# Kernel tuning notes

Hardware: AMD Instinct MI355X
Metric: run time of the kernel (lower is better)

The kernel has to match this reference:

```python
import jax, jax.numpy as jnp
import numpy as np

B, CIN, CP, H, W = 64, 256, 128, 32, 32
EPS = 1e-5


def conv1x1(x, w, b):
    # x: [B,C,H,W], w: [O,C], b: [O]
    return jnp.einsum('bchw,oc->bohw', x, w) + b[None, :, None, None]


def batchnorm(x, g, beta):
    # training-mode BatchNorm2d (batch stats over B,H,W; biased variance)
    m = x.mean(axis=(0, 2, 3), keepdims=True)
    v = x.var(axis=(0, 2, 3), keepdims=True)
    return (x - m) * jax.lax.rsqrt(v + EPS) * g[None, :, None, None] + beta[None, :, None, None]


def setup_inputs() -> dict:
    key = jax.random.key(0)
    ks = jax.random.split(key, 5)
    s = 0.05  # keep pre-softmax logits in a sane range
    d = {
        'x': jax.random.normal(ks[0], (B, CIN, H, W), jnp.float32),
        'theta_w': jax.random.normal(ks[1], (CP, CIN), jnp.float32) * s,
        'theta_b': jnp.zeros((CP,), jnp.float32),
        'theta_g': jnp.ones((CP,), jnp.float32),
        'theta_beta': jnp.zeros((CP,), jnp.float32),
        'phi_w': jax.random.normal(ks[2], (CP, CIN), jnp.float32) * s,
        'phi_b': jnp.zeros((CP,), jnp.float32),
        'phi_g': jnp.ones((CP,), jnp.float32),
        'phi_beta': jnp.zeros((CP,), jnp.float32),
        'gamma_w': jax.random.normal(ks[3], (CP, CIN), jnp.float32) * s,
        'gamma_b': jnp.zeros((CP,), jnp.float32),
        'gamma_g': jnp.ones((CP,), jnp.float32),
        'gamma_beta': jnp.zeros((CP,), jnp.float32),
        'omega_w': jax.random.normal(ks[4], (CIN, CP), jnp.float32) * s,
        'omega_b': jnp.zeros((CIN,), jnp.float32),
        'omega_g': jnp.ones((CIN,), jnp.float32),
        'omega_beta': jnp.zeros((CIN,), jnp.float32),
    }
    return d


def reference(x, theta_w, theta_b, theta_g, theta_beta,
              phi_w, phi_b, phi_g, phi_beta,
              gamma_w, gamma_b, gamma_g, gamma_beta,
              omega_w, omega_b, omega_g, omega_beta):
    b, c, h, w = x.shape
    n = h * w
    t = batchnorm(conv1x1(x, theta_w, theta_b), theta_g, theta_beta).reshape(b, -1, n)  # [B,CP,N]
    p = batchnorm(conv1x1(x, phi_w, phi_b), phi_g, phi_beta).reshape(b, -1, n)          # [B,CP,N]
    g = batchnorm(conv1x1(x, gamma_w, gamma_b), gamma_g, gamma_beta).reshape(b, -1, n)  # [B,CP,N]
    # attention = t^T @ p : [B,N,N]
    attn = jnp.einsum('bcn,bcm->bnm', t, p)
    # whole-matrix softmax (normalize over all N*N entries per batch element)
    attn = jax.nn.softmax(attn.reshape(b, -1), axis=1).reshape(b, n, n)
    # sat = attn @ g^T, kept channels-first: [B,CP,N]
    sat = jnp.einsum('bnm,bcm->bcn', attn, g).reshape(b, -1, h, w)
    sat = batchnorm(conv1x1(sat, omega_w, omega_b), omega_g, omega_beta)
    return x + sat
```

## Files before the change

### kernel.cpp

```cpp
#include <hip/hip_runtime.h>
#include <cstdio>


typedef __attribute__((ext_vector_type(4))) float f32x4;
typedef __attribute__((ext_vector_type(8))) short short8;
typedef __attribute__((ext_vector_type(4))) unsigned short u16x4;
typedef __attribute__((ext_vector_type(8))) unsigned short u16x8;
typedef __attribute__((ext_vector_type(4))) int i32x4;

static constexpr float CEXP = 40.0f;
static constexpr float LOG2E = 1.4426950408889634f;

static constexpr long OFF_WST  = 0;
static constexpr long OFF_VEC  = 147456;
static constexpr long OFF_R1   = 148608;
static constexpr long OFF_R2   = 149376;
static constexpr long OFF_ZS   = 149888;
static constexpr long OFF_SC1  = 149952;
static constexpr long OFF_SH1  = 150336;
static constexpr long OFF_SC2  = 150720;
static constexpr long OFF_SH2  = 150976;
static constexpr long OFF_INVZ = 151232;
static constexpr long OFF_OM   = 151296;
static constexpr long OFF_X    = 262144;
static constexpr long OFF_Y    = OFF_X + 16777216;
static constexpr long OFF_C    = OFF_Y + 25165824;
static constexpr long OFF_D    = OFF_C + 4194304;
static constexpr long WS_FLOATS = OFF_D + 4194304;

__device__ __forceinline__ unsigned short f2bf(float f) {
    union { float f; unsigned u; } x; x.f = f;
    unsigned r = x.u + 0x7FFF + ((x.u >> 16) & 1);
    return (unsigned short)(r >> 16);
}
__device__ __forceinline__ float bf2f(unsigned short h) {
    union { unsigned u; float f; } x; x.u = ((unsigned)h) << 16; return x.f;
}
__device__ __forceinline__ void glds16(const void* g, void* l) {
    __builtin_amdgcn_global_load_lds(
        (const __attribute__((address_space(1))) unsigned int*)g,
        (__attribute__((address_space(3))) unsigned int*)l, 16, 0, 0);
}

__global__ void zero_n(float* p, int n) {
    int i = blockIdx.x * 256 + threadIdx.x;
    if (i < n) p[i] = 0.f;
}

__global__ void invz_kernel(const float* zs, float* invz) {
    int i = threadIdx.x;
    if (i < 64) invz[i] = 1.0f / zs[i];
}

__global__ void stack_params(const float* tw, const float* tb, const float* tg, const float* tbe,
                             const float* pw, const float* pb, const float* pg, const float* pbe,
                             const float* gw, const float* gb, const float* gg, const float* gbe,
                             const float* ow,
                             unsigned short* Wsp, float* vecs, unsigned short* omB) {
    int i = blockIdx.x * 256 + threadIdx.x;
    if (i < 98304) {
        int o = i >> 8, c = i & 255;
        float v = (o < 128) ? tw[o * 256 + c] : (o < 256) ? pw[(o - 128) * 256 + c]
                                                          : gw[(o - 256) * 256 + c];
        unsigned short hi = f2bf(v);
        unsigned short lo = f2bf(v - bf2f(hi));
        Wsp[(long)o * 768 + c] = hi;
        Wsp[(long)o * 768 + 256 + c] = lo;
        Wsp[(long)o * 768 + 512 + c] = hi;
    }
    if (i < 32768) omB[i] = f2bf(ow[i]);
    if (i < 384) {
        float b  = (i < 128) ? tb[i]  : (i < 256) ? pb[i - 128]  : gb[i - 256];
        float g  = (i < 128) ? tg[i]  : (i < 256) ? pg[i - 128]  : gg[i - 256];
        float be = (i < 128) ? tbe[i] : (i < 256) ? pbe[i - 128] : gbe[i - 256];
        vecs[i] = b; vecs[384 + i] = g; vecs[768 + i] = be;
    }
}

__global__ __launch_bounds__(256) void transpose_x(const float* __restrict__ x,
                                                   unsigned short* __restrict__ xs) {
    __shared__ float t[64][68];
    const int b = blockIdx.z, c0 = blockIdx.y * 64, n0 = blockIdx.x * 64;
    const int tid = threadIdx.x;
#pragma unroll
    for (int p = 0; p < 4; ++p) {
        int i = tid + p * 256;
        int c = i >> 4, n4 = (i & 15) << 2;
        f32x4 v = *(const f32x4*)&x[((long)b * 256 + c0 + c) * 1024 + n0 + n4];
        *(f32x4*)&t[c][n4] = v;
    }
    __syncthreads();
#pragma unroll
    for (int p = 0; p < 4; ++p) {
        int i = tid + p * 256;
        int n = i >> 4, c4 = (i & 15) << 2;
        u16x4 h, l;
#pragma unroll
        for (int j = 0; j < 4; ++j) {
            float v = t[c4 + j][n];
            unsigned short hh = f2bf(v);
            h[j] = hh;
            l[j] = f2bf(v - bf2f(hh));
        }
        long o = ((long)b * 1024 + n0 + n) * 512 + c0 + c4;
        *(u16x4*)&xs[o] = h;
        *(u16x4*)&xs[o + 256] = l;
    }
}

template <int NT, bool OUT_BF16, bool HAS_CBIAS, bool CSTAT, bool EXPZ>
__global__ __launch_bounds__(512) void mgemm8(
    int gx, int gy,
    const unsigned short* __restrict__ A, long aBatch, long aOff, int lda,
    int athr, int adlo, int adhi,
    const unsigned short* __restrict__ B, long bBatch, long bOff, int ldb,
    int bthr, int bdlo, int bdhi,
    void* __restrict__ Cq, long cBatch, int ldc,
    const float* __restrict__ bias, float* __restrict__ stats, int statStride,
    float* __restrict__ zsum) {
    constexpr int AU = 256 * 64;
    constexpr int BU = 128 * 64;
    constexpr int BUFU = AU + BU;
    __shared__ unsigned short lds[3 * BUFU];

    const int nwg = gridDim.x, bid = blockIdx.x;
    const int wk = ((bid & 7) * (nwg >> 3)) + (bid >> 3);
    const int bx = wk % gx;
    const int byz = wk / gx;
    const int by = byz % gy;
    const int z = byz / gy;

    const int tid = threadIdx.x;
    const int wave = tid >> 6, lane = tid & 63;
    const int wm = wave >> 1, wn = wave & 1;
    const int lr = lane & 15, lg = lane >> 4;
    const int m0 = by * 256, n0 = bx * 128;
    const long aB = aOff + (long)z * aBatch;
    const long bB = bOff + (long)z * bBatch;
    const int grow = lane >> 3, gq = lane & 7;

    f32x4 acc[4][4];
#pragma unroll
    for (int i = 0; i < 4; ++i)
#pragma unroll
        for (int j = 0; j < 4; ++j) acc[i][j] = (f32x4){0.f, 0.f, 0.f, 0.f};

    auto stageA = [&](int buf, int kt, int t) {
        const int ka = (kt < athr ? kt + adlo : kt + adhi);
        int seg = wave + t * 8;
        int row = seg * 8 + grow;
        glds16(A + aB + (long)(m0 + row) * lda + ka + ((gq ^ (row & 7)) << 3),
               &lds[buf + seg * 512]);
    };
    auto stageB = [&](int buf, int kt, int t) {
        const int kb = (kt < bthr ? kt + bdlo : kt + bdhi);
        int seg = wave + t * 8;
        int row = seg * 8 + grow;
        glds16(B + bB + (long)(n0 + row) * ldb + kb + ((gq ^ (row & 7)) << 3),
               &lds[buf + AU + seg * 512]);
    };
    auto stage_all = [&](int buf, int kt) {
#pragma unroll
        for (int t = 0; t < 4; ++t) stageA(buf, kt, t);
#pragma unroll
        for (int t = 0; t < 2; ++t) stageB(buf, kt, t);
    };

    stage_all(0, 0);
    if (NT > 1) stage_all(BUFU, 64);

#pragma unroll
    for (int t = 0; t < NT; ++t) {
        const unsigned bb = (unsigned)(((t % 3) * BUFU) * 2);
        if (t + 1 < NT) asm volatile("s_waitcnt vmcnt(6)" ::: "memory");
        else            asm volatile("s_waitcnt vmcnt(0)" ::: "memory");
        asm volatile("s_barrier" ::: "memory");
        const int sbuf = ((t + 2) % 3) * BUFU;
        const int skt = (t + 2) * 64;
#pragma unroll
        for (int p = 0; p < 2; ++p) {
            i32x4 a4[4], b4[4];
#pragma unroll
            for (int mi = 0; mi < 4; ++mi) {
                unsigned r = (unsigned)(wm * 64 + mi * 16 + lr);
                unsigned ad = bb + r * 128 + ((unsigned)(((p << 2) | lg) ^ (r & 7)) << 4);
                asm volatile("ds_read_b128 %0, %1" : "=v"(a4[mi]) : "v"(ad));
            }
#pragma unroll
            for (int ni = 0; ni < 4; ++ni) {
                unsigned r = (unsigned)(wn * 64 + ni * 16 + lr);
                unsigned ad = bb + (unsigned)(AU * 2) + r * 128 +
                              ((unsigned)(((p << 2) | lg) ^ (r & 7)) << 4);
                asm volatile("ds_read_b128 %0, %1" : "=v"(b4[ni]) : "v"(ad));
            }
            if (t + 2 < NT) {
                if (p == 0) { stageA(sbuf, skt, 0); stageA(sbuf, skt, 1); stageA(sbuf, skt, 2); }
                else        { stageA(sbuf, skt, 3); stageB(sbuf, skt, 0); stageB(sbuf, skt, 1); }
            }
            asm volatile("s_waitcnt lgkmcnt(0)" ::: "memory");
            __builtin_amdgcn_sched_barrier(0);
            __builtin_amdgcn_s_setprio(1);
#pragma unroll
            for (int ni = 0; ni < 4; ++ni) {
                short8 bh = __builtin_bit_cast(short8, b4[ni]);
#pragma unroll
                for (int mi = 0; mi < 4; ++mi)
                    acc[mi][ni] = __builtin_amdgcn_mfma_f32_16x16x32_bf16(
                        __builtin_bit_cast(short8, a4[mi]), bh, acc[mi][ni], 0, 0, 0);
            }
            __builtin_amdgcn_s_setprio(0);
            if (p == 0) asm volatile("s_barrier" ::: "memory");
        }
    }

    float cb[4];
#pragma unroll
    for (int ni = 0; ni < 4; ++ni)
        cb[ni] = HAS_CBIAS ? bias[n0 + wn * 64 + ni * 16 + lr] : 0.0f;

    if constexpr (OUT_BF16) {
        __syncthreads();
        unsigned short* tileH = lds;
        float zacc = 0.f;
#pragma unroll
        for (int mi = 0; mi < 4; ++mi) {
            const int lrow = wm * 64 + mi * 16 + lg * 4;
#pragma unroll
            for (int ni = 0; ni < 4; ++ni) {
                const int cl = wn * 64 + ni * 16 + lr;
                f32x4 v = acc[mi][ni] + (f32x4){cb[ni], cb[ni], cb[ni], cb[ni]};
#pragma unroll
                for (int j = 0; j < 4; ++j) {
                    unsigned short o;
                    if constexpr (EXPZ) {
                        float e = exp2f((v[j] - CEXP) * LOG2E);
                        o = f2bf(e);
                        zacc += bf2f(o);
                    } else {
                        o = f2bf(v[j]);
                    }
                    tileH[(lrow + j) * 128 + cl] = o;
                }
            }
        }
        __syncthreads();
#pragma unroll
        for (int i = tid; i < 256 * 128 / 8; i += 512) {
            int row = i >> 4, c8 = (i & 15) << 3;
            u16x8 vv = *(const u16x8*)&tileH[row * 128 + c8];
            *(u16x8*)&((unsigned short*)Cq)[(long)z * cBatch + (long)(m0 + row) * ldc + n0 + c8] = vv;
        }
        if constexpr (EXPZ) {
            __syncthreads();
            float* red = (float*)lds;
            red[tid] = zacc;
            __syncthreads();
            for (int o = 256; o > 0; o >>= 1) {
                if (tid < o) red[tid] += red[tid + o];
                __syncthreads();
            }
            if (tid == 0) atomicAdd(&zsum[z], red[0]);
        }
    } else {
        float* tileF = (float*)lds;
        float scol[4] = {0.f, 0.f, 0.f, 0.f}, s2col[4] = {0.f, 0.f, 0.f, 0.f};
#pragma unroll
        for (int pass = 0; pass < 2; ++pass) {
            __syncthreads();
            if ((wm >> 1) == pass) {
#pragma unroll
                for (int mi = 0; mi < 4; ++mi) {
                    const int lrow = (wm & 1) * 64 + mi * 16 + lg * 4;
#pragma unroll
                    for (int ni = 0; ni < 4; ++ni) {
                        const int cl = wn * 64 + ni * 16 + lr;
                        f32x4 v = acc[mi][ni] + (f32x4){cb[ni], cb[ni], cb[ni], cb[ni]};
                        if constexpr (CSTAT) {
                            scol[ni] += v[0] + v[1] + v[2] + v[3];
                            s2col[ni] += v[0] * v[0] + v[1] * v[1] + v[2] * v[2] + v[3] * v[3];
                        }
#pragma unroll
                        for (int j = 0; j < 4; ++j) tileF[(lrow + j) * 128 + cl] = v[j];
                    }
                }
            }
            __syncthreads();
#pragma unroll
            for (int i = tid; i < 128 * 128 / 4; i += 512) {
                int row = i >> 5, c4 = (i & 31) << 2;
                f32x4 vv = *(const f32x4*)&tileF[row * 128 + c4];
                *(f32x4*)&((float*)Cq)[(long)z * cBatch +
                                       (long)(m0 + pass * 128 + row) * ldc + n0 + c4] = vv;
            }
        }
        if constexpr (CSTAT) {
#pragma unroll
            for (int ni = 0; ni < 4; ++ni) {
                float a = scol[ni], b2 = s2col[ni];
                a += __shfl_xor(a, 16); a += __shfl_xor(a, 32);
                b2 += __shfl_xor(b2, 16); b2 += __shfl_xor(b2, 32);
                if (lg == 0) {
                    const int col = n0 + wn * 64 + ni * 16 + lr;
                    atomicAdd(&stats[col], a);
                    atomicAdd(&stats[statStride + col], b2);
                }
            }
        }
    }
}

template <int NF, int KTOT, bool OUT_BF16, bool HAS_BIAS, bool HAS_CBIAS, bool HAS_SCALE,
          bool RSTAT, bool CSTAT, bool EXPZ>
__global__ __launch_bounds__(256) void mgemm(
    int gx, int gy,
    const unsigned short* __restrict__ A, long aBatch, long aOff, int lda,
    int athr, int adlo, int adhi,
    const unsigned short* __restrict__ B, long bBatch, long bOff, int ldb,
    int bthr, int bdlo, int bdhi,
    void* __restrict__ Cq, long cBatch, int ldc,
    const float* __restrict__ bias, const float* __restrict__ bscale,
    float* __restrict__ stats, int statStride, float* __restrict__ zsum) {
    constexpr int AU = 128 * 32;
    constexpr int BU = NF * 32 * 32;
    constexpr int BUFU = AU + BU;
    constexpr int S = KTOT / 32;
    constexpr int LPS = 2 + NF / 2;
    constexpr int COLS = NF * 32;
    __shared__ unsigned short lds[4 * BUFU];

    const int nwg = gridDim.x;
    const int bid = blockIdx.x;
    const int wk = ((bid & 7) * (nwg >> 3)) + (bid >> 3);
    const int bx = wk % gx;
    const int byz = wk / gx;
    const int by = byz % gy;
    const int z = byz / gy;

    const int tid = threadIdx.x;
    const int wave = tid >> 6, lane = tid & 63;
    const int wm = wave >> 1, wn = wave & 1;
    const int lr = lane & 15, lg = lane >> 4;
    const int m0 = by * 128, n0 = bx * COLS;
    const long aB = aOff + (long)z * aBatch;
    const long bB = bOff + (long)z * bBatch;
    const int srow = lane >> 2;
    const int sq   = lane & 3;

    f32x4 acc[4][NF];
#pragma unroll
    for (int i = 0; i < 4; ++i)
#pragma unroll
        for (int j = 0; j < NF; ++j) acc[i][j] = (f32x4){0.f, 0.f, 0.f, 0.f};

    auto stage = [&](int bufu, int kt) {
        const int ka = (kt < athr ? kt + adlo : kt + adhi);
        const int kb = (kt < bthr ? kt + bdlo : kt + bdhi);
#pragma unroll
        for (int t = 0; t < 2; ++t) {
            int seg = wave + t * 4;
            int row = seg * 16 + srow;
            int gq = sq ^ ((row >> 1) & 3);
            glds16(A + aB + (long)(m0 + row) * lda + ka + gq * 8, &lds[bufu + seg * 512]);
        }
#pragma unroll
        for (int t = 0; t < NF / 2; ++t) {
            int seg = wave + t * 4;
            int row = seg * 16 + srow;
            int gq = sq ^ ((row >> 1) & 3);
            glds16(B + bB + (long)(n0 + row) * ldb + kb + gq * 8, &lds[bufu + AU + seg * 512]);
        }
    };

    stage(0, 0);
    stage(BUFU, 32);
    stage(2 * BUFU, 64);

#pragma unroll
    for (int s = 0; s < S; ++s) {
        const int bufu = (s & 3) * BUFU;
        const unsigned bb = (unsigned)(bufu * 2);
        const int rem = (S - 1 - s) < 2 ? (S - 1 - s) : 2;
        if (rem == 2)      asm volatile("s_waitcnt vmcnt(%0)" ::"i"(2 * LPS) : "memory");
        else if (rem == 1) asm volatile("s_waitcnt vmcnt(%0)" ::"i"(LPS) : "memory");
        else               asm volatile("s_waitcnt vmcnt(0)" ::: "memory");
        asm volatile("s_barrier" ::: "memory");
        i32x4 a4[4], b4[NF];
#pragma unroll
        for (int mi = 0; mi < 4; ++mi) {
            unsigned r = (unsigned)(wm * 64 + mi * 16 + lr);
            unsigned ad = bb + r * 64 + ((unsigned)(lg ^ ((r >> 1) & 3)) * 16);
            asm volatile("ds_read_b128 %0, %1" : "=v"(a4[mi]) : "v"(ad));
        }
#pragma unroll
        for (int ni = 0; ni < NF; ++ni) {
            unsigned r = (unsigned)(wn * NF * 16 + ni * 16 + lr);
            unsigned ad = bb + (unsigned)(AU * 2) + r * 64 + ((unsigned)(lg ^ ((r >> 1) & 3)) * 16);
            asm volatile("ds_read_b128 %0, %1" : "=v"(b4[ni]) : "v"(ad));
        }
        if (s + 3 < S) stage(((s + 3) & 3) * BUFU, (s + 3) * 32);
        asm volatile("s_waitcnt lgkmcnt(0)" ::: "memory");
        __builtin_amdgcn_sched_barrier(0);
        __builtin_amdgcn_s_setprio(1);
#pragma unroll
        for (int ni = 0; ni < NF; ++ni) {
            short8 bh = __builtin_bit_cast(short8, b4[ni]);
#pragma unroll
            for (int mi = 0; mi < 4; ++mi)
                acc[mi][ni] = __builtin_amdgcn_mfma_f32_16x16x32_bf16(
                    __builtin_bit_cast(short8, a4[mi]), bh, acc[mi][ni], 0, 0, 0);
        }
        __builtin_amdgcn_s_setprio(0);
    }

    __syncthreads();
    const float sc = HAS_SCALE ? bscale[z] : 1.0f;
    float zacc = 0.f;
    float scol[NF], s2col[NF];
    if constexpr (CSTAT) {
#pragma unroll
        for (int ni = 0; ni < NF; ++ni) { scol[ni] = 0.f; s2col[ni] = 0.f; }
    }
    unsigned short* tileH = lds;
    float* tileF = (float*)lds;
#pragma unroll
    for (int mi = 0; mi < 4; ++mi) {
        const int mrow = m0 + wm * 64 + mi * 16 + lg * 4;
        const int lrow = wm * 64 + mi * 16 + lg * 4;
        f32x4 bi = (f32x4){0.f, 0.f, 0.f, 0.f};
        if constexpr (HAS_BIAS) bi = *(const f32x4*)&bias[mrow];
        f32x4 s = (f32x4){0.f, 0.f, 0.f, 0.f}, s2 = s;
#pragma unroll
        for (int ni = 0; ni < NF; ++ni) {
            const int cl = wn * NF * 16 + ni * 16 + lr;
            f32x4 v = acc[mi][ni] * sc + bi;
            if constexpr (HAS_CBIAS) {
                float bc = bias[n0 + cl];
                v += (f32x4){bc, bc, bc, bc};
            }
            if constexpr (RSTAT) { s += v; s2 += v * v; }
            if constexpr (CSTAT) {
                scol[ni] += v[0] + v[1] + v[2] + v[3];
                s2col[ni] += v[0] * v[0] + v[1] * v[1] + v[2] * v[2] + v[3] * v[3];
            }
            if constexpr (OUT_BF16) {
#pragma unroll
                for (int j = 0; j < 4; ++j) {
                    unsigned short o;
                    if constexpr (EXPZ) {
                        float e = exp2f((v[j] - CEXP) * LOG2E);
                        o = f2bf(e);
                        zacc += bf2f(o);
                    } else {
                        o = f2bf(v[j]);
                    }
                    tileH[(lrow + j) * COLS + cl] = o;
                }
            } else {
#pragma unroll
                for (int j = 0; j < 4; ++j) tileF[(lrow + j) * COLS + cl] = v[j];
            }
        }
        if constexpr (RSTAT) {
#pragma unroll
            for (int m = 1; m < 16; m <<= 1) {
#pragma unroll
                for (int r = 0; r < 4; ++r) {
                    s[r] += __shfl_xor(s[r], m);
                    s2[r] += __shfl_xor(s2[r], m);
                }
            }
            if (lr == 0) {
#pragma unroll
                for (int r = 0; r < 4; ++r) {
                    atomicAdd(&stats[mrow + r], s[r]);
                    atomicAdd(&stats[statStride + mrow + r], s2[r]);
                }
            }
        }
    }
    if constexpr (CSTAT) {
#pragma unroll
        for (int ni = 0; ni < NF; ++ni) {
            float a = scol[ni], b2 = s2col[ni];
            a += __shfl_xor(a, 16); a += __shfl_xor(a, 32);
            b2 += __shfl_xor(b2, 16); b2 += __shfl_xor(b2, 32);
            if (lg == 0) {
                const int col = n0 + wn * NF * 16 + ni * 16 + lr;
                atomicAdd(&stats[col], a);
                atomicAdd(&stats[statStride + col], b2);
            }
        }
    }
    __syncthreads();
    if constexpr (OUT_BF16) {
#pragma unroll
        for (int i = tid; i < 128 * COLS / 8; i += 256) {
            int row = i / (COLS / 8), c8 = (i % (COLS / 8)) * 8;
            u16x8 vv = *(const u16x8*)&tileH[row * COLS + c8];
            *(u16x8*)&((unsigned short*)Cq)[(long)z * cBatch + (long)(m0 + row) * ldc + n0 + c8] = vv;
        }
    } else {
#pragma unroll
        for (int i = tid; i < 128 * COLS / 4; i += 256) {
            int row = i / (COLS / 4), c4 = (i % (COLS / 4)) * 4;
            f32x4 vv = *(const f32x4*)&tileF[row * COLS + c4];
            *(f32x4*)&((float*)Cq)[(long)z * cBatch + (long)(m0 + row) * ldc + n0 + c4] = vv;
        }
    }
    if constexpr (EXPZ) {
        __syncthreads();
        float* red = (float*)lds;
        red[tid] = zacc;
        __syncthreads();
        for (int o = 128; o > 0; o >>= 1) {
            if (tid < o) red[tid] += red[tid + o];
            __syncthreads();
        }
        if (tid == 0) atomicAdd(&zsum[z], red[0]);
    }
}

__global__ void finalize_stats(const float* __restrict__ raw, int n, int stride,
                               const float* __restrict__ g, const float* __restrict__ beta,
                               float* __restrict__ osc, float* __restrict__ osh) {
    int ch = blockIdx.x * 256 + threadIdx.x;
    if (ch < n) {
        double mean = (double)raw[ch] / 65536.0;
        double var = (double)raw[stride + ch] / 65536.0 - mean * mean;
        double s = (double)g[ch] / sqrt(var + 1e-5);
        osc[ch] = (float)s;
        osh[ch] = (float)((double)beta[ch] - mean * s);
    }
}

__global__ __launch_bounds__(256) void norm_tp(const float* __restrict__ YT,
                                               const float* __restrict__ sc,
                                               const float* __restrict__ sh,
                                               unsigned short* __restrict__ tps) {
    const long total = 64L * 1024 * 64;
    for (long idx = (long)blockIdx.x * 256 + threadIdx.x; idx < total;
         idx += (long)gridDim.x * 256) {
        long row = idx >> 6;
        int cg = (int)(idx & 63) << 2;
        f32x4 v = *(const f32x4*)&YT[row * 384 + cg];
        f32x4 scv = *(const f32x4*)&sc[cg];
        f32x4 shv = *(const f32x4*)&sh[cg];
        v = v * scv + shv;
        u16x4 h, l;
#pragma unroll
        for (int j = 0; j < 4; ++j) {
            unsigned short hh = f2bf(v[j]);
            h[j] = hh;
            l[j] = f2bf(v[j] - bf2f(hh));
        }
        long rb = row * 512;
        if (cg < 128) {
            *(u16x4*)&tps[rb + cg] = h;
            *(u16x4*)&tps[rb + 128 + cg] = l;
        } else {
            *(u16x4*)&tps[rb + 128 + cg] = h;
            *(u16x4*)&tps[rb + 256 + cg] = l;
        }
    }
}

__global__ __launch_bounds__(256) void norm_g(const float* __restrict__ YT,
                                              const float* __restrict__ sc,
                                              const float* __restrict__ sh,
                                              unsigned short* __restrict__ g) {
    __shared__ float t[64][68];
    const int b = blockIdx.z, c0 = blockIdx.y * 64, n0 = blockIdx.x * 64;
    const int tid = threadIdx.x;
#pragma unroll
    for (int p = 0; p < 4; ++p) {
        int i = tid + p * 256;
        int n = i >> 4, c4 = (i & 15) << 2;
        f32x4 v = *(const f32x4*)&YT[((long)b * 1024 + n0 + n) * 384 + 256 + c0 + c4];
        f32x4 scv = *(const f32x4*)&sc[256 + c0 + c4];
        f32x4 shv = *(const f32x4*)&sh[256 + c0 + c4];
        v = v * scv + shv;
        *(f32x4*)&t[n][c4] = v;
    }
    __syncthreads();
#pragma unroll
    for (int p = 0; p < 4; ++p) {
        int i = tid + p * 256;
        int c = i >> 4, n4 = (i & 15) << 2;
        u16x4 o;
#pragma unroll
        for (int j = 0; j < 4; ++j) o[j] = f2bf(t[n4 + j][c]);
        *(u16x4*)&g[((long)b * 128 + c0 + c) * 1024 + n0 + n4] = o;
    }
}

__global__ __launch_bounds__(256) void final_kernel(const float* __restrict__ x,
                                                    const float* __restrict__ out0T,
                                                    const float* __restrict__ sc,
                                                    const float* __restrict__ sh,
                                                    float* __restrict__ out) {
    __shared__ float t[64][68];
    const int b = blockIdx.z, oc0 = blockIdx.y * 64, n0 = blockIdx.x * 64;
    const int tid = threadIdx.x;
#pragma unroll
    for (int p = 0; p < 4; ++p) {
        int i = tid + p * 256;
        int n = i >> 4, c4 = (i & 15) << 2;
        f32x4 v = *(const f32x4*)&out0T[((long)b * 1024 + n0 + n) * 256 + oc0 + c4];
        *(f32x4*)&t[n][c4] = v;
    }
    __syncthreads();
#pragma unroll
    for (int p = 0; p < 4; ++p) {
        int i = tid + p * 256;
        int oc = i >> 4, n4 = (i & 15) << 2;
        const float scv = sc[oc0 + oc], shv = sh[oc0 + oc];
        long o = ((long)b * 256 + oc0 + oc) * 1024 + n0 + n4;
        f32x4 xv = *(const f32x4*)&x[o];
        f32x4 v;
#pragma unroll
        for (int j = 0; j < 4; ++j) v[j] = xv[j] + t[n4 + j][oc] * scv + shv;
        *(f32x4*)&out[o] = v;
    }
}

extern "C" void kernel_launch(void* const* d_in, const int* in_sizes, int n_in,
                              void* d_out, int out_size, void* d_ws, size_t ws_size,
                              hipStream_t stream) {
    const float* x        = (const float*)d_in[0];
    const float* theta_w  = (const float*)d_in[1];
    const float* theta_b  = (const float*)d_in[2];
    const float* theta_g  = (const float*)d_in[3];
    const float* theta_be = (const float*)d_in[4];
    const float* phi_w    = (const float*)d_in[5];
    const float* phi_b    = (const float*)d_in[6];
    const float* phi_g    = (const float*)d_in[7];
    const float* phi_be   = (const float*)d_in[8];
    const float* gamma_w  = (const float*)d_in[9];
    const float* gamma_b  = (const float*)d_in[10];
    const float* gamma_g  = (const float*)d_in[11];
    const float* gamma_be = (const float*)d_in[12];
    const float* omega_w  = (const float*)d_in[13];
    const float* omega_b  = (const float*)d_in[14];
    const float* omega_g  = (const float*)d_in[15];
    const float* omega_be = (const float*)d_in[16];
    float* out = (float*)d_out;

    const size_t need = (size_t)WS_FLOATS * 4;
    if (ws_size < need) {
        fprintf(stderr, "kernel_launch: ws_size %zu < needed %zu\n", ws_size, need);
        return;
    }
    float* ws = (float*)d_ws;
    unsigned short* Wsp = (unsigned short*)(ws + OFF_WST);
    float* vecs = ws + OFF_VEC;
    float* r1   = ws + OFF_R1;
    float* r2   = ws + OFF_R2;
    float* zs   = ws + OFF_ZS;
    float* sc1  = ws + OFF_SC1;
    float* sh1  = ws + OFF_SH1;
    float* sc2  = ws + OFF_SC2;
    float* sh2  = ws + OFF_SH2;
    float* invz = ws + OFF_INVZ;
    unsigned short* omB = (unsigned short*)(ws + OFF_OM);
    unsigned short* xs  = (unsigned short*)(ws + OFF_X);
    unsigned short* tps = (unsigned short*)(ws + OFF_X);
    float* out0T        = ws + OFF_X;
    float* YT           = ws + OFF_Y;
    unsigned short* P   = (unsigned short*)(ws + OFF_Y);
    unsigned short* g   = (unsigned short*)(ws + OFF_C);
    unsigned short* satT= (unsigned short*)(ws + OFF_D);

    const int NOMAP = 1 << 30;

    zero_n<<<6, 256, 0, stream>>>(r1, 1344);
    stack_params<<<384, 256, 0, stream>>>(theta_w, theta_b, theta_g, theta_be,
                                          phi_w, phi_b, phi_g, phi_be,
                                          gamma_w, gamma_b, gamma_g, gamma_be,
                                          omega_w, Wsp, vecs, omB);
    transpose_x<<<dim3(16, 4, 64), 256, 0, stream>>>(x, xs);

    mgemm8<12, false, true, true, false><<<768, 512, 0, stream>>>(
        3, 256,
        xs, 0, 0, 512, 256, 0, -256,
        Wsp, 0, 0, 768, NOMAP, 0, 0,
        YT, 0, 384, vecs, r1, 384, nullptr);
    finalize_stats<<<2, 256, 0, stream>>>(r1, 384, 384, vecs + 384, vecs + 768, sc1, sh1);

    norm_tp<<<4096, 256, 0, stream>>>(YT, sc1, sh1, tps);
    norm_g<<<dim3(16, 2, 64), 256, 0, stream>>>(YT, sc1, sh1, g);

    for (int c = 0; c < 2; ++c) {
        const long b0 = (long)c * 32;
        mgemm8<6, true, false, false, true><<<1024, 512, 0, stream>>>(
            8, 4,
            tps, 524288, b0 * 524288, 512, 128, 0, -128,
            tps, 524288, b0 * 524288, 512, 256, 256, 0,
            P, 1048576, 1024, nullptr, nullptr, 0, zs + b0);

        mgemm<2, 1024, true, false, false, false, false, false, false><<<512, 256, 0, stream>>>(
            2, 8,
            P, 1048576, 0, 1024, NOMAP, 0, 0,
            g, 131072, b0 * 131072, 1024, NOMAP, 0, 0,
            satT + b0 * 131072, 131072, 128, nullptr, nullptr, nullptr, 0, nullptr);
    }
    invz_kernel<<<1, 64, 0, stream>>>(zs, invz);

    mgemm<4, 128, false, false, true, true, false, true, false><<<1024, 256, 0, stream>>>(
        2, 8,
        satT, 131072, 0, 128, NOMAP, 0, 0,
        omB, 0, 0, 128, NOMAP, 0, 0,
        out0T, 262144, 256, omega_b, invz, r2, 256, nullptr);
    finalize_stats<<<1, 256, 0, stream>>>(r2, 256, 256, omega_g, omega_be, sc2, sh2);

    final_kernel<<<dim3(16, 4, 64), 256, 0, stream>>>(x, out0T, sc2, sh2, out);
}
```

Measured before the change: 344.8 us.

## Unify GEMMs on 256x128 mgemm8, drop batch chunking, transpose omega output layout

Removes the older 128-row mgemm kernel and routes the attention-times-g and omega GEMMs through the larger-tile mgemm8, which gains row-bias, scale and row-statistics epilogue options. The two half-batch passes become one launch, so the full P matrix is written to a larger workspace. The omega projection now writes channel-major output, which lets the final residual kernel become a plain elementwise grid-stride loop with no LDS transpose. The aim is fewer launches, better tile reuse and cheaper final fusion, at the cost of more workspace memory and a larger P intermediate living in memory at once.

```diff
diff --git a/kernel.cpp b/kernel.cpp
--- a/kernel.cpp
+++ b/kernel.cpp
@@ -24,7 +24,7 @@
 static constexpr long OFF_OM   = 151296;
 static constexpr long OFF_X    = 262144;
 static constexpr long OFF_Y    = OFF_X + 16777216;
-static constexpr long OFF_C    = OFF_Y + 25165824;
+static constexpr long OFF_C    = OFF_Y + 33554432;
 static constexpr long OFF_D    = OFF_C + 4194304;
 static constexpr long WS_FLOATS = OFF_D + 4194304;
 
@@ -108,7 +108,8 @@
     }
 }
 
-template <int NT, bool OUT_BF16, bool HAS_CBIAS, bool CSTAT, bool EXPZ>
+template <int NT, bool OUT_BF16, bool HAS_RBIAS, bool HAS_CBIAS, bool HAS_SCALE,
+          bool RSTAT, bool CSTAT, bool EXPZ>
 __global__ __launch_bounds__(512) void mgemm8(
     int gx, int gy,
     const unsigned short* __restrict__ A, long aBatch, long aOff, int lda,
@@ -116,8 +117,8 @@
     const unsigned short* __restrict__ B, long bBatch, long bOff, int ldb,
     int bthr, int bdlo, int bdhi,
     void* __restrict__ Cq, long cBatch, int ldc,
-    const float* __restrict__ bias, float* __restrict__ stats, int statStride,
-    float* __restrict__ zsum) {
+    const float* __restrict__ bias, const float* __restrict__ bscale,
+    float* __restrict__ stats, int statStride, float* __restrict__ zsum) {
     constexpr int AU = 256 * 64;
     constexpr int BU = 128 * 64;
     constexpr int BUFU = AU + BU;
@@ -213,10 +214,61 @@
         }
     }
 
-    float cb[4];
-#pragma unroll
-    for (int ni = 0; ni < 4; ++ni)
-        cb[ni] = HAS_CBIAS ? bias[n0 + wn * 64 + ni * 16 + lr] : 0.0f;
+    const float sc = HAS_SCALE ? bscale[z] : 1.0f;
+#pragma unroll
+    for (int mi = 0; mi < 4; ++mi) {
+        const int mrow = m0 + wm * 64 + mi * 16 + lg * 4;
+        f32x4 rb = (f32x4){0.f, 0.f, 0.f, 0.f};
+        if constexpr (HAS_RBIAS) rb = *(const f32x4*)&bias[mrow];
+#pragma unroll
+        for (int ni = 0; ni < 4; ++ni) {
+            float cbv = HAS_CBIAS ? bias[n0 + wn * 64 + ni * 16 + lr] : 0.0f;
+            acc[mi][ni] = acc[mi][ni] * sc + rb + (f32x4){cbv, cbv, cbv, cbv};
+        }
+    }
+    if constexpr (RSTAT) {
+#pragma unroll
+        for (int mi = 0; mi < 4; ++mi) {
+            const int mrow = m0 + wm * 64 + mi * 16 + lg * 4;
+            f32x4 s = (f32x4){0.f, 0.f, 0.f, 0.f}, s2 = s;
+#pragma unroll
+            for (int ni = 0; ni < 4; ++ni) { s += acc[mi][ni]; s2 += acc[mi][ni] * acc[mi][ni]; }
+#pragma unroll
+            for (int m = 1; m < 16; m <<= 1) {
+#pragma unroll
+                for (int r = 0; r < 4; ++r) {
+                    s[r] += __shfl_xor(s[r], m);
+                    s2[r] += __shfl_xor(s2[r], m);
+                }
+            }
+            if (lr == 0) {
+#pragma unroll
+                for (int r = 0; r < 4; ++r) {
+                    atomicAdd(&stats[mrow + r], s[r]);
+                    atomicAdd(&stats[statStride + mrow + r], s2[r]);
+                }
+            }
+        }
+    }
+    if constexpr (CSTAT) {
+#pragma unroll
+        for (int ni = 0; ni < 4; ++ni) {
+            float a = 0.f, b2 = 0.f;
+#pragma unroll
+            for (int mi = 0; mi < 4; ++mi) {
+                f32x4 v = acc[mi][ni];
+                a += v[0] + v[1] + v[2] + v[3];
+                b2 += v[0] * v[0] + v[1] * v[1] + v[2] * v[2] + v[3] * v[3];
+            }
+            a += __shfl_xor(a, 16); a += __shfl_xor(a, 32);
+            b2 += __shfl_xor(b2, 16); b2 += __shfl_xor(b2, 32);
+            if (lg == 0) {
+                const int col = n0 + wn * 64 + ni * 16 + lr;
+                atomicAdd(&stats[col], a);
+                atomicAdd(&stats[statStride + col], b2);
+            }
+        }
+    }
 
     if constexpr (OUT_BF16) {
         __syncthreads();
@@ -228,7 +280,7 @@
 #pragma unroll
             for (int ni = 0; ni < 4; ++ni) {
                 const int cl = wn * 64 + ni * 16 + lr;
-                f32x4 v = acc[mi][ni] + (f32x4){cb[ni], cb[ni], cb[ni], cb[ni]};
+                f32x4 v = acc[mi][ni];
 #pragma unroll
                 for (int j = 0; j < 4; ++j) {
                     unsigned short o;
@@ -263,7 +315,6 @@
         }
     } else {
         float* tileF = (float*)lds;
-        float scol[4] = {0.f, 0.f, 0.f, 0.f}, s2col[4] = {0.f, 0.f, 0.f, 0.f};
 #pragma unroll
         for (int pass = 0; pass < 2; ++pass) {
             __syncthreads();
@@ -274,13 +325,8 @@
 #pragma unroll
                     for (int ni = 0; ni < 4; ++ni) {
                         const int cl = wn * 64 + ni * 16 + lr;
-                        f32x4 v = acc[mi][ni] + (f32x4){cb[ni], cb[ni], cb[ni], cb[ni]};
-                        if constexpr (CSTAT) {
-                            scol[ni] += v[0] + v[1] + v[2] + v[3];
-                            s2col[ni] += v[0] * v[0] + v[1] * v[1] + v[2] * v[2] + v[3] * v[3];
-                        }
-#pragma unroll
-                        for (int j = 0; j < 4; ++j) tileF[(lrow + j) * 128 + cl] = v[j];
+#pragma unroll
+                        for (int j = 0; j < 4; ++j) tileF[(lrow + j) * 128 + cl] = acc[mi][ni][j];
                     }
                 }
             }
@@ -293,230 +339,6 @@
                                        (long)(m0 + pass * 128 + row) * ldc + n0 + c4] = vv;
             }
         }
-        if constexpr (CSTAT) {
-#pragma unroll
-            for (int ni = 0; ni < 4; ++ni) {
-                float a = scol[ni], b2 = s2col[ni];
-                a += __shfl_xor(a, 16); a += __shfl_xor(a, 32);
-                b2 += __shfl_xor(b2, 16); b2 += __shfl_xor(b2, 32);
-                if (lg == 0) {
-                    const int col = n0 + wn * 64 + ni * 16 + lr;
-                    atomicAdd(&stats[col], a);
-                    atomicAdd(&stats[statStride + col], b2);
-                }
-            }
-        }
-    }
-}
-
-template <int NF, int KTOT, bool OUT_BF16, bool HAS_BIAS, bool HAS_CBIAS, bool HAS_SCALE,
-          bool RSTAT, bool CSTAT, bool EXPZ>
-__global__ __launch_bounds__(256) void mgemm(
-    int gx, int gy,
-    const unsigned short* __restrict__ A, long aBatch, long aOff, int lda,
-    int athr, int adlo, int adhi,
-    const unsigned short* __restrict__ B, long bBatch, long bOff, int ldb,
-    int bthr, int bdlo, int bdhi,
-    void* __restrict__ Cq, long cBatch, int ldc,
-    const float* __restrict__ bias, const float* __restrict__ bscale,
-    float* __restrict__ stats, int statStride, float* __restrict__ zsum) {
-    constexpr int AU = 128 * 32;
-    constexpr int BU = NF * 32 * 32;
-    constexpr int BUFU = AU + BU;
-    constexpr int S = KTOT / 32;
-    constexpr int LPS = 2 + NF / 2;
-    constexpr int COLS = NF * 32;
-    __shared__ unsigned short lds[4 * BUFU];
-
-    const int nwg = gridDim.x;
-    const int bid = blockIdx.x;
-    const int wk = ((bid & 7) * (nwg >> 3)) + (bid >> 3);
-    const int bx = wk % gx;
-    const int byz = wk / gx;
-    const int by = byz % gy;
-    const int z = byz / gy;
-
-    const int tid = threadIdx.x;
-    const int wave = tid >> 6, lane = tid & 63;
-    const int wm = wave >> 1, wn = wave & 1;
-    const int lr = lane & 15, lg = lane >> 4;
-    const int m0 = by * 128, n0 = bx * COLS;
-    const long aB = aOff + (long)z * aBatch;
-    const long bB = bOff + (long)z * bBatch;
-    const int srow = lane >> 2;
-    const int sq   = lane & 3;
-
-    f32x4 acc[4][NF];
-#pragma unroll
-    for (int i = 0; i < 4; ++i)
-#pragma unroll
-        for (int j = 0; j < NF; ++j) acc[i][j] = (f32x4){0.f, 0.f, 0.f, 0.f};
-
-    auto stage = [&](int bufu, int kt) {
-        const int ka = (kt < athr ? kt + adlo : kt + adhi);
-        const int kb = (kt < bthr ? kt + bdlo : kt + bdhi);
-#pragma unroll
-        for (int t = 0; t < 2; ++t) {
-            int seg = wave + t * 4;
-            int row = seg * 16 + srow;
-            int gq = sq ^ ((row >> 1) & 3);
-            glds16(A + aB + (long)(m0 + row) * lda + ka + gq * 8, &lds[bufu + seg * 512]);
-        }
-#pragma unroll
-        for (int t = 0; t < NF / 2; ++t) {
-            int seg = wave + t * 4;
-            int row = seg * 16 + srow;
-            int gq = sq ^ ((row >> 1) & 3);
-            glds16(B + bB + (long)(n0 + row) * ldb + kb + gq * 8, &lds[bufu + AU + seg * 512]);
-        }
-    };
-
-    stage(0, 0);
-    stage(BUFU, 32);
-    stage(2 * BUFU, 64);
-
-#pragma unroll
-    for (int s = 0; s < S; ++s) {
-        const int bufu = (s & 3) * BUFU;
-        const unsigned bb = (unsigned)(bufu * 2);
-        const int rem = (S - 1 - s) < 2 ? (S - 1 - s) : 2;
-        if (rem == 2)      asm volatile("s_waitcnt vmcnt(%0)" ::"i"(2 * LPS) : "memory");
-        else if (rem == 1) asm volatile("s_waitcnt vmcnt(%0)" ::"i"(LPS) : "memory");
-        else               asm volatile("s_waitcnt vmcnt(0)" ::: "memory");
-        asm volatile("s_barrier" ::: "memory");
-        i32x4 a4[4], b4[NF];
-#pragma unroll
-        for (int mi = 0; mi < 4; ++mi) {
-            unsigned r = (unsigned)(wm * 64 + mi * 16 + lr);
-            unsigned ad = bb + r * 64 + ((unsigned)(lg ^ ((r >> 1) & 3)) * 16);
-            asm volatile("ds_read_b128 %0, %1" : "=v"(a4[mi]) : "v"(ad));
-        }
-#pragma unroll
-        for (int ni = 0; ni < NF; ++ni) {
-            unsigned r = (unsigned)(wn * NF * 16 + ni * 16 + lr);
-            unsigned ad = bb + (unsigned)(AU * 2) + r * 64 + ((unsigned)(lg ^ ((r >> 1) & 3)) * 16);
-            asm volatile("ds_read_b128 %0, %1" : "=v"(b4[ni]) : "v"(ad));
-        }
-        if (s + 3 < S) stage(((s + 3) & 3) * BUFU, (s + 3) * 32);
-        asm volatile("s_waitcnt lgkmcnt(0)" ::: "memory");
-        __builtin_amdgcn_sched_barrier(0);
-        __builtin_amdgcn_s_setprio(1);
-#pragma unroll
-        for (int ni = 0; ni < NF; ++ni) {
-            short8 bh = __builtin_bit_cast(short8, b4[ni]);
-#pragma unroll
-            for (int mi = 0; mi < 4; ++mi)
-                acc[mi][ni] = __builtin_amdgcn_mfma_f32_16x16x32_bf16(
-                    __builtin_bit_cast(short8, a4[mi]), bh, acc[mi][ni], 0, 0, 0);
-        }
-        __builtin_amdgcn_s_setprio(0);
-    }
-
-    __syncthreads();
-    const float sc = HAS_SCALE ? bscale[z] : 1.0f;
-    float zacc = 0.f;
-    float scol[NF], s2col[NF];
-    if constexpr (CSTAT) {
-#pragma unroll
-        for (int ni = 0; ni < NF; ++ni) { scol[ni] = 0.f; s2col[ni] = 0.f; }
-    }
-    unsigned short* tileH = lds;
-    float* tileF = (float*)lds;
-#pragma unroll
-    for (int mi = 0; mi < 4; ++mi) {
-        const int mrow = m0 + wm * 64 + mi * 16 + lg * 4;
-        const int lrow = wm * 64 + mi * 16 + lg * 4;
-        f32x4 bi = (f32x4){0.f, 0.f, 0.f, 0.f};
-        if constexpr (HAS_BIAS) bi = *(const f32x4*)&bias[mrow];
-        f32x4 s = (f32x4){0.f, 0.f, 0.f, 0.f}, s2 = s;
-#pragma unroll
-        for (int ni = 0; ni < NF; ++ni) {
-            const int cl = wn * NF * 16 + ni * 16 + lr;
-            f32x4 v = acc[mi][ni] * sc + bi;
-            if constexpr (HAS_CBIAS) {
-                float bc = bias[n0 + cl];
-                v += (f32x4){bc, bc, bc, bc};
-            }
-            if constexpr (RSTAT) { s += v; s2 += v * v; }
-            if constexpr (CSTAT) {
-                scol[ni] += v[0] + v[1] + v[2] + v[3];
-                s2col[ni] += v[0] * v[0] + v[1] * v[1] + v[2] * v[2] + v[3] * v[3];
-            }
-            if constexpr (OUT_BF16) {
-#pragma unroll
-                for (int j = 0; j < 4; ++j) {
-                    unsigned short o;
-                    if constexpr (EXPZ) {
-                        float e = exp2f((v[j] - CEXP) * LOG2E);
-                        o = f2bf(e);
-                        zacc += bf2f(o);
-                    } else {
-                        o = f2bf(v[j]);
-                    }
-                    tileH[(lrow + j) * COLS + cl] = o;
-                }
-            } else {
-#pragma unroll
-                for (int j = 0; j < 4; ++j) tileF[(lrow + j) * COLS + cl] = v[j];
-            }
-        }
-        if constexpr (RSTAT) {
-#pragma unroll
-            for (int m = 1; m < 16; m <<= 1) {
-#pragma unroll
-                for (int r = 0; r < 4; ++r) {
-                    s[r] += __shfl_xor(s[r], m);
-                    s2[r] += __shfl_xor(s2[r], m);
-                }
-            }
-            if (lr == 0) {
-#pragma unroll
-                for (int r = 0; r < 4; ++r) {
-                    atomicAdd(&stats[mrow + r], s[r]);
-                    atomicAdd(&stats[statStride + mrow + r], s2[r]);
-                }
-            }
-        }
-    }
-    if constexpr (CSTAT) {
-#pragma unroll
-        for (int ni = 0; ni < NF; ++ni) {
-            float a = scol[ni], b2 = s2col[ni];
-            a += __shfl_xor(a, 16); a += __shfl_xor(a, 32);
-            b2 += __shfl_xor(b2, 16); b2 += __shfl_xor(b2, 32);
-            if (lg == 0) {
-                const int col = n0 + wn * NF * 16 + ni * 16 + lr;
-                atomicAdd(&stats[col], a);
-                atomicAdd(&stats[statStride + col], b2);
-            }
-        }
-    }
-    __syncthreads();
-    if constexpr (OUT_BF16) {
-#pragma unroll
-        for (int i = tid; i < 128 * COLS / 8; i += 256) {
-            int row = i / (COLS / 8), c8 = (i % (COLS / 8)) * 8;
-            u16x8 vv = *(const u16x8*)&tileH[row * COLS + c8];
-            *(u16x8*)&((unsigned short*)Cq)[(long)z * cBatch + (long)(m0 + row) * ldc + n0 + c8] = vv;
-        }
-    } else {
-#pragma unroll
-        for (int i = tid; i < 128 * COLS / 4; i += 256) {
-            int row = i / (COLS / 4), c4 = (i % (COLS / 4)) * 4;
-            f32x4 vv = *(const f32x4*)&tileF[row * COLS + c4];
-            *(f32x4*)&((float*)Cq)[(long)z * cBatch + (long)(m0 + row) * ldc + n0 + c4] = vv;
-        }
-    }
-    if constexpr (EXPZ) {
-        __syncthreads();
-        float* red = (float*)lds;
-        red[tid] = zacc;
-        __syncthreads();
-        for (int o = 128; o > 0; o >>= 1) {
-            if (tid < o) red[tid] += red[tid + o];
-            __syncthreads();
-        }
-        if (tid == 0) atomicAdd(&zsum[z], red[0]);
     }
 }
 
@@ -594,32 +416,25 @@
 }
 
 __global__ __launch_bounds__(256) void final_kernel(const float* __restrict__ x,
-                                                    const float* __restrict__ out0T,
+                                                    const float* __restrict__ out0,
                                                     const float* __restrict__ sc,
                                                     const float* __restrict__ sh,
                                                     float* __restrict__ out) {
-    __shared__ float t[64][68];
-    const int b = blockIdx.z, oc0 = blockIdx.y * 64, n0 = blockIdx.x * 64;
-    const int tid = threadIdx.x;
-#pragma unroll
-    for (int p = 0; p < 4; ++p) {
-        int i = tid + p * 256;
-        int n = i >> 4, c4 = (i & 15) << 2;
-        f32x4 v = *(const f32x4*)&out0T[((long)b * 1024 + n0 + n) * 256 + oc0 + c4];
-        *(f32x4*)&t[n][c4] = v;
-    }
-    __syncthreads();
-#pragma unroll
-    for (int p = 0; p < 4; ++p) {
-        int i = tid + p * 256;
-        int oc = i >> 4, n4 = (i & 15) << 2;
-        const float scv = sc[oc0 + oc], shv = sh[oc0 + oc];
-        long o = ((long)b * 256 + oc0 + oc) * 1024 + n0 + n4;
-        f32x4 xv = *(const f32x4*)&x[o];
+    const long total4 = 64L * 256 * 256;
+    for (long idx = (long)blockIdx.x * 256 + threadIdx.x; idx < total4;
+         idx += (long)gridDim.x * 256) {
+        long e = idx << 2;
+        int n = (int)(e & 1023);
+        long t = e >> 10;
+        int oc = (int)(t & 255);
+        long b = t >> 8;
+        f32x4 xv = *(const f32x4*)&x[e];
+        f32x4 ov = *(const f32x4*)&out0[(long)oc * 65536 + b * 1024 + n];
+        const float scv = sc[oc], shv = sh[oc];
         f32x4 v;
 #pragma unroll
-        for (int j = 0; j < 4; ++j) v[j] = xv[j] + t[n4 + j][oc] * scv + shv;
-        *(f32x4*)&out[o] = v;
+        for (int j = 0; j < 4; ++j) v[j] = xv[j] + ov[j] * scv + shv;
+        *(f32x4*)&out[e] = v;
     }
 }
 
@@ -664,9 +479,9 @@
     unsigned short* omB = (unsigned short*)(ws + OFF_OM);
     unsigned short* xs  = (unsigned short*)(ws + OFF_X);
     unsigned short* tps = (unsigned short*)(ws + OFF_X);
-    float* out0T        = ws + OFF_X;
     float* YT           = ws + OFF_Y;
     unsigned short* P   = (unsigned short*)(ws + OFF_Y);
+    float* out0         = ws + OFF_Y;
     unsigned short* g   = (unsigned short*)(ws + OFF_C);
     unsigned short* satT= (unsigned short*)(ws + OFF_D);
 
@@ -679,38 +494,35 @@
                                           omega_w, Wsp, vecs, omB);
     transpose_x<<<dim3(16, 4, 64), 256, 0, stream>>>(x, xs);
 
-    mgemm8<12, false, true, true, false><<<768, 512, 0, stream>>>(
+    mgemm8<12, false, false, true, false, false, true, false><<<768, 512, 0, stream>>>(
         3, 256,
         xs, 0, 0, 512, 256, 0, -256,
         Wsp, 0, 0, 768, NOMAP, 0, 0,
-        YT, 0, 384, vecs, r1, 384, nullptr);
+        YT, 0, 384, vecs, nullptr, r1, 384, nullptr);
     finalize_stats<<<2, 256, 0, stream>>>(r1, 384, 384, vecs + 384, vecs + 768, sc1, sh1);
 
     norm_tp<<<4096, 256, 0, stream>>>(YT, sc1, sh1, tps);
     norm_g<<<dim3(16, 2, 64), 256, 0, stream>>>(YT, sc1, sh1, g);
 
-    for (int c = 0; c < 2; ++c) {
-        const long b0 = (long)c * 32;
-        mgemm8<6, true, false, false, true><<<1024, 512, 0, stream>>>(
-            8, 4,
-            tps, 524288, b0 * 524288, 512, 128, 0, -128,
-            tps, 524288, b0 * 524288, 512, 256, 256, 0,
-            P, 1048576, 1024, nullptr, nullptr, 0, zs + b0);
-
-        mgemm<2, 1024, true, false, false, false, false, false, false><<<512, 256, 0, stream>>>(
-            2, 8,
-            P, 1048576, 0, 1024, NOMAP, 0, 0,
-            g, 131072, b0 * 131072, 1024, NOMAP, 0, 0,
-            satT + b0 * 131072, 131072, 128, nullptr, nullptr, nullptr, 0, nullptr);
-    }
+    mgemm8<6, true, false, false, false, false, false, true><<<2048, 512, 0, stream>>>(
+        8, 4,
+        tps, 524288, 0, 512, 128, 0, -128,
+        tps, 524288, 0, 512, 256, 256, 0,
+        P, 1048576, 1024, nullptr, nullptr, nullptr, 0, zs);
     invz_kernel<<<1, 64, 0, stream>>>(zs, invz);
 
-    mgemm<4, 128, false, false, true, true, false, true, false><<<1024, 256, 0, stream>>>(
-        2, 8,
-        satT, 131072, 0, 128, NOMAP, 0, 0,
+    mgemm8<16, true, false, false, true, false, false, false><<<256, 512, 0, stream>>>(
+        1, 4,
+        P, 1048576, 0, 1024, NOMAP, 0, 0,
+        g, 131072, 0, 1024, NOMAP, 0, 0,
+        satT, 131072, 128, nullptr, invz, nullptr, 0, nullptr);
+
+    mgemm8<2, false, true, false, false, true, false, false><<<512, 512, 0, stream>>>(
+        512, 1,
         omB, 0, 0, 128, NOMAP, 0, 0,
-        out0T, 262144, 256, omega_b, invz, r2, 256, nullptr);
+        satT, 0, 0, 128, NOMAP, 0, 0,
+        out0, 0, 65536, omega_b, nullptr, r2, 256, nullptr);
     finalize_stats<<<1, 256, 0, stream>>>(r2, 256, 256, omega_g, omega_be, sc2, sh2);
 
-    final_kernel<<<dim3(16, 4, 64), 256, 0, stream>>>(x, out0T, sc2, sh2, out);
-}
+    final_kernel<<<2048, 256, 0, stream>>>(x, out0, sc2, sh2, out);
+}
```

After: 415.8 us. +20.6%, slower.
